# Optimization experiments

Measured on AMD Instinct MI355X. Metric: run time of the kernel, lower is better.

## Reference

```python
import jax, jax.numpy as jnp
import numpy as np

N = 100000   # nodes
E = 1600000  # edges
D = 128      # feature dim
C = 32       # n classes (logits dim)
LN_EPS = 1e-5   # torch LayerNorm default eps
LOG_EPS = 1e-9  # numerical floor inside logs


def setup_inputs() -> dict:
    key = jax.random.key(0)
    ks = jax.random.split(key, 8)
    h = jax.random.normal(ks[0], (N, D), jnp.float32)
    logits = jax.random.normal(ks[1], (N, C), jnp.float32)
    old_z = jax.random.uniform(ks[2], (N,), jnp.float32)
    norm = jax.random.uniform(ks[3], (N, 1), jnp.float32)  # degree norm per node
    tau_1 = jax.random.uniform(ks[4], (1,), jnp.float32)
    tau_2 = jax.random.uniform(ks[5], (1,), jnp.float32)
    src = jax.random.randint(ks[6], (E,), 0, N, jnp.int32)
    dst = jax.random.randint(ks[7], (E,), 0, N, jnp.int32)
    return dict(h=h, logits=logits, old_z=old_z, norm=norm,
                tau_1=tau_1, tau_2=tau_2, src=src, dst=dst)


def _layernorm_over_nodes(x):
    # LayerNorm(N, elementwise_affine=False) applied to a length-N vector:
    # normalize over the entire node dimension.
    mu = jnp.mean(x)
    var = jnp.mean(jnp.square(x - mu))
    return (x - mu) * jax.lax.rsqrt(var + LN_EPS)


def reference(h, logits, old_z, norm, tau_1, tau_2, src, dst):
    # --- message pass 1: adaptive_reduce_func over neighbor logits ---
    probs = jax.nn.softmax(logits, axis=-1)                      # [N,C]
    ones = jnp.ones((src.shape[0],), h.dtype)
    deg = jax.ops.segment_sum(ones, dst, num_segments=N)          # in-degree [N]
    sum_p = jax.ops.segment_sum(probs[src], dst, num_segments=N)  # [N,C]
    mean_p = sum_p / jnp.maximum(deg, 1.0)[:, None]               # neighborhood consensus
    log_self = jnp.log(probs + LOG_EPS)
    log_mean = jnp.log(mean_p + LOG_EPS)
    f1 = jnp.sum(probs * (log_self - log_mean), axis=-1)          # KL(self || mean-neighbor)
    f2 = -jnp.sum(mean_p * log_mean, axis=-1)                     # entropy of consensus
    has_nb = deg > 0  # DGL leaves zero-in-degree nodes at 0
    f1 = jnp.where(has_nb, f1, 0.0)
    f2 = jnp.where(has_nb, f2, 0.0)

    # --- gating (shared_tau=True path) ---
    z = jax.nn.sigmoid(-(_layernorm_over_nodes(f1) - tau_1)) \
      * jax.nn.sigmoid(-(_layernorm_over_nodes(f2) - tau_2))      # [N]
    gate = jnp.minimum(old_z, z)

    # --- message pass 2: sum-aggregate neighbor features ---
    agg = jax.ops.segment_sum(h[src], dst, num_segments=N)        # [N,D]
    normagg = jax.nn.relu(agg * norm)
    new_h = h + gate[:, None] * normagg
    return new_h, z
```

## Files before the change

### kernel.cpp

```cpp
#include <hip/hip_runtime.h>
#include <math.h>

#define CN 32
#define DN 128
#define BKT_SHIFT 9
#define BKT_NODES 512
#define CHUNK 8192
#define MAXBKT 1024
#define DCAP 12288

__global__ void k_softmax(const float* __restrict__ logits, float* __restrict__ probs, int N) {
    int t = blockIdx.x * blockDim.x + threadIdx.x;
    int node = t >> 5, c = t & 31;
    if (node >= N) return;
    float l = logits[node * CN + c];
    float m = l;
    #pragma unroll
    for (int o = 16; o; o >>= 1) m = fmaxf(m, __shfl_xor(m, o, 32));
    float e = __expf(l - m);
    float s = e;
    #pragma unroll
    for (int o = 16; o; o >>= 1) s += __shfl_xor(s, o, 32);
    probs[node * CN + c] = e / s;
}

__global__ void k_part_hist(const int* __restrict__ dst, int* __restrict__ M,
                            int E, int NBKT) {
    __shared__ int hist[MAXBKT];
    int t = threadIdx.x;
    for (int j = t; j < NBKT; j += 256) hist[j] = 0;
    __syncthreads();
    int ebeg = blockIdx.x * CHUNK;
    #pragma unroll
    for (int k = 0; k < CHUNK / 256; ++k) {
        int e = ebeg + k * 256 + t;
        if (e < E) atomicAdd(&hist[dst[e] >> BKT_SHIFT], 1);
    }
    __syncthreads();
    int* row = M + (size_t)blockIdx.x * NBKT;
    for (int j = t; j < NBKT; j += 256) row[j] = hist[j];
}

__global__ void k_part_scan(int* __restrict__ M, int* __restrict__ bbase,
                            int NCH, int NBKT, int E) {
    __shared__ int wsum[16], wpre[16];
    __shared__ int carry;
    int t = threadIdx.x, ln = t & 63, wv = t >> 6;
    if (t == 0) carry = 0;
    __syncthreads();
    int L = NCH * NBKT;
    for (int base = 0; base < L; base += 1024) {
        int k = base + t;
        int idx = 0, v = 0;
        if (k < L) {
            int b = k / NCH, ch = k - b * NCH;
            idx = ch * NBKT + b;
            v = M[idx];
        }
        int incl = v;
        #pragma unroll
        for (int o = 1; o < 64; o <<= 1) { int u = __shfl_up(incl, o, 64); if (ln >= o) incl += u; }
        if (ln == 63) wsum[wv] = incl;
        __syncthreads();
        if (t == 0) {
            int r = carry;
            #pragma unroll
            for (int w = 0; w < 16; ++w) { wpre[w] = r; r += wsum[w]; }
            carry = r;
        }
        __syncthreads();
        if (k < L) M[idx] = wpre[wv] + incl - v;
        __syncthreads();
    }
    for (int b = t; b < NBKT; b += 1024) bbase[b] = M[b];
    if (t == 0) bbase[NBKT] = E;
}

__global__ void k_part_scatter(const int* __restrict__ src, const int* __restrict__ dst,
                               const int* __restrict__ M, int* __restrict__ part,
                               int E, int NBKT) {
    __shared__ int cur[MAXBKT];
    int t = threadIdx.x;
    const int* row = M + (size_t)blockIdx.x * NBKT;
    for (int j = t; j < NBKT; j += 256) cur[j] = row[j];
    __syncthreads();
    int ebeg = blockIdx.x * CHUNK;
    #pragma unroll
    for (int k = 0; k < CHUNK / 256; ++k) {
        int e = ebeg + k * 256 + t;
        if (e < E) {
            int d = dst[e];
            int b = d >> BKT_SHIFT;
            int p = atomicAdd(&cur[b], 1);
            part[p] = ((d & (BKT_NODES - 1)) << 17) | src[e];
        }
    }
}

__global__ void k_bucket_csr(int* __restrict__ part, const int* __restrict__ bbase,
                             int* __restrict__ cnt, int* __restrict__ off, int N) {
    __shared__ int sbuf[DCAP];
    __shared__ int hcnt[BKT_NODES];
    __shared__ int wsum[8], wpre[8];
    int t = threadIdx.x, ln = t & 63, wv = t >> 6;
    int b = blockIdx.x;
    int lo = bbase[b], hi = bbase[b + 1];
    int n = hi - lo;
    if (n > DCAP) n = DCAP;
    for (int e = t; e < n; e += BKT_NODES) sbuf[e] = part[lo + e];
    hcnt[t] = 0;
    __syncthreads();
    for (int e = t; e < n; e += BKT_NODES) atomicAdd(&hcnt[sbuf[e] >> 17], 1);
    __syncthreads();
    int v = hcnt[t];
    int incl = v;
    #pragma unroll
    for (int o = 1; o < 64; o <<= 1) { int u = __shfl_up(incl, o, 64); if (ln >= o) incl += u; }
    if (ln == 63) wsum[wv] = incl;
    __syncthreads();
    if (t == 0) {
        int r = 0;
        #pragma unroll
        for (int w = 0; w < 8; ++w) { wpre[w] = r; r += wsum[w]; }
    }
    __syncthreads();
    int excl = wpre[wv] + incl - v;
    int g = b * BKT_NODES + t;
    if (g < N) { cnt[g] = v; off[g] = lo + excl; }
    hcnt[t] = excl;
    __syncthreads();
    for (int e = t; e < n; e += BKT_NODES) {
        int pk = sbuf[e];
        int p = atomicAdd(&hcnt[pk >> 17], 1);
        part[lo + p] = pk & 0x1FFFF;
    }
}

__global__ void k_fused(const float* __restrict__ probs, const int* __restrict__ off,
                        const int* __restrict__ cnt, const int* __restrict__ eidx,
                        float* __restrict__ f1buf, float* __restrict__ f2buf,
                        double* __restrict__ pbuf,
                        const float* __restrict__ h, float* __restrict__ aggout,
                        int N, int NBF) {
    if ((int)blockIdx.x < NBF) {
        int t = blockIdx.x * blockDim.x + threadIdx.x;
        int i = t >> 5, c = t & 31;
        float f1 = 0.f, f2 = 0.f;
        if (i < N) {
            int beg = off[i], dg = cnt[i];
            float sum = 0.f;
            for (int base = 0; base < dg; base += 16) {
                int rem = dg - base;
                int lim = rem < 16 ? rem : 16;
                int myi = (c < lim) ? eidx[beg + base + c] : 0;
                #pragma unroll
                for (int j = 0; j < 16; ++j) {
                    int s = __shfl(myi, j, 32);
                    float v = probs[(size_t)s * CN + c];
                    sum += (j < rem) ? v : 0.f;
                }
            }
            float f1c = 0.f, f2c = 0.f;
            if (dg > 0) {
                float p = probs[(size_t)i * CN + c];
                float mp = sum / (float)dg;
                float lm = logf(mp + 1e-9f);
                f1c = p * (logf(p + 1e-9f) - lm);
                f2c = -mp * lm;
            }
            #pragma unroll
            for (int o = 16; o; o >>= 1) { f1c += __shfl_xor(f1c, o, 32); f2c += __shfl_xor(f2c, o, 32); }
            if (c == 0) { f1buf[i] = f1c; f2buf[i] = f2c; f1 = f1c; f2 = f2c; }
        }
        double v0 = f1, v1 = (double)f1 * f1, v2 = f2, v3 = (double)f2 * f2;
        #pragma unroll
        for (int o = 32; o; o >>= 1) {
            v0 += __shfl_down(v0, o, 64);
            v1 += __shfl_down(v1, o, 64);
            v2 += __shfl_down(v2, o, 64);
            v3 += __shfl_down(v3, o, 64);
        }
        __shared__ double sh[4][4];
        int wave = threadIdx.x >> 6, lane = threadIdx.x & 63;
        if (lane == 0) { sh[0][wave] = v0; sh[1][wave] = v1; sh[2][wave] = v2; sh[3][wave] = v3; }
        __syncthreads();
        if (threadIdx.x == 0) {
            double a = 0, b = 0, c2 = 0, d = 0;
            #pragma unroll
            for (int w = 0; w < 4; ++w) { a += sh[0][w]; b += sh[1][w]; c2 += sh[2][w]; d += sh[3][w]; }
            double* p = pbuf + (size_t)blockIdx.x * 4;
            p[0] = a; p[1] = b; p[2] = c2; p[3] = d;
        }
    } else {
        int bb = blockIdx.x - NBF;
        int t = bb * blockDim.x + threadIdx.x;
        int i = t >> 6, ln = t & 63;
        if (i >= N) return;
        int beg = off[i], dg = cnt[i];
        const float2* h2 = (const float2*)h;
        float ax = 0.f, ay = 0.f;
        for (int base = 0; base < dg; base += 16) {
            int rem = dg - base;
            int lim = rem < 16 ? rem : 16;
            int myi = (ln < lim) ? eidx[beg + base + ln] : 0;
            #pragma unroll
            for (int j = 0; j < 16; ++j) {
                int s = __shfl(myi, j, 64);
                float2 v = h2[(size_t)s * 64 + ln];
                bool use = j < rem;
                ax += use ? v.x : 0.f;
                ay += use ? v.y : 0.f;
            }
        }
        float2 r; r.x = ax; r.y = ay;
        ((float2*)aggout)[(size_t)i * 64 + ln] = r;
    }
}

__global__ void k_redstats(const double* __restrict__ pbuf, double* __restrict__ stats, int nblk) {
    int t = threadIdx.x;
    double a = 0, b = 0, c = 0, d = 0;
    for (int k = t; k < nblk; k += blockDim.x) {
        const double* p = pbuf + (size_t)k * 4;
        a += p[0]; b += p[1]; c += p[2]; d += p[3];
    }
    #pragma unroll
    for (int o = 32; o; o >>= 1) {
        a += __shfl_down(a, o, 64);
        b += __shfl_down(b, o, 64);
        c += __shfl_down(c, o, 64);
        d += __shfl_down(d, o, 64);
    }
    __shared__ double sh[4][16];
    int wv = t >> 6, ln = t & 63;
    if (ln == 0) { sh[0][wv] = a; sh[1][wv] = b; sh[2][wv] = c; sh[3][wv] = d; }
    __syncthreads();
    if (t == 0) {
        double s0 = 0, s1 = 0, s2 = 0, s3 = 0;
        int nw = blockDim.x >> 6;
        for (int w = 0; w < nw; ++w) { s0 += sh[0][w]; s1 += sh[1][w]; s2 += sh[2][w]; s3 += sh[3][w]; }
        stats[0] = s0; stats[1] = s1; stats[2] = s2; stats[3] = s3;
    }
}

__global__ void k_z_ep(const float* __restrict__ f1buf, const float* __restrict__ f2buf,
                       const double* __restrict__ stats, const float* __restrict__ old_z,
                       const float* __restrict__ tau1, const float* __restrict__ tau2,
                       const float* __restrict__ h, const float* __restrict__ norm,
                       float* __restrict__ out, float* __restrict__ z_out, int N) {
    int t = blockIdx.x * blockDim.x + threadIdx.x;
    int i = t >> 5, c = t & 31;
    if (i >= N) return;
    double invN = 1.0 / (double)N;
    float mu1 = (float)(stats[0] * invN);
    float var1 = (float)(stats[1] * invN) - mu1 * mu1;
    float is1 = rsqrtf(var1 + 1e-5f);
    float mu2 = (float)(stats[2] * invN);
    float var2 = (float)(stats[3] * invN) - mu2 * mu2;
    float is2 = rsqrtf(var2 + 1e-5f);
    float a = (f1buf[i] - mu1) * is1;
    float b = (f2buf[i] - mu2) * is2;
    float z = (1.f / (1.f + __expf(a - tau1[0]))) * (1.f / (1.f + __expf(b - tau2[0])));
    if (c == 0) z_out[i] = z;
    float g = fminf(old_z[i], z);
    float nm = norm[i];
    float4 av = ((const float4*)out)[(size_t)i * 32 + c];
    float4 hv = ((const float4*)h)[(size_t)i * 32 + c];
    float4 r;
    r.x = hv.x + g * fmaxf(av.x * nm, 0.f);
    r.y = hv.y + g * fmaxf(av.y * nm, 0.f);
    r.z = hv.z + g * fmaxf(av.z * nm, 0.f);
    r.w = hv.w + g * fmaxf(av.w * nm, 0.f);
    ((float4*)out)[(size_t)i * 32 + c] = r;
}

extern "C" void kernel_launch(void* const* d_in, const int* in_sizes, int n_in,
                              void* d_out, int out_size, void* d_ws, size_t ws_size,
                              hipStream_t stream) {
    const float* h      = (const float*)d_in[0];
    const float* logits = (const float*)d_in[1];
    const float* old_z  = (const float*)d_in[2];
    const float* norm   = (const float*)d_in[3];
    const float* tau1   = (const float*)d_in[4];
    const float* tau2   = (const float*)d_in[5];
    const int*   src    = (const int*)d_in[6];
    const int*   dst    = (const int*)d_in[7];
    const int N = in_sizes[2];
    const int E = in_sizes[6];

    float* out   = (float*)d_out;
    float* z_out = out + (size_t)N * DN;

    const int B = 256;
    const int NBF  = (N * CN + B - 1) / B;
    const int NG   = (N * 64 + B - 1) / B;
    const int NBKT = (N + BKT_NODES - 1) >> BKT_SHIFT;
    const int NCH  = (E + CHUNK - 1) / CHUNK;

    char*   ws    = (char*)d_ws;
    double* stats = (double*)ws;
    int*    cnt   = (int*)(ws + 64);
    int*    off   = cnt + N;
    int*    bbase = off + N;
    int*    M     = bbase + MAXBKT + 8;
    int*    eidx  = M + (size_t)NCH * NBKT;
    float*  probs = (float*)(eidx + E);
    float*  f1buf = probs + (size_t)N * CN;
    float*  f2buf = f1buf + N;
    double* pbuf  = (double*)(((size_t)(f2buf + N) + 15) & ~(size_t)15);

    k_softmax<<<(N * CN + B - 1) / B, B, 0, stream>>>(logits, probs, N);

    k_part_hist<<<NCH, 256, 0, stream>>>(dst, M, E, NBKT);
    k_part_scan<<<1, 1024, 0, stream>>>(M, bbase, NCH, NBKT, E);
    k_part_scatter<<<NCH, 256, 0, stream>>>(src, dst, M, eidx, E, NBKT);
    k_bucket_csr<<<NBKT, BKT_NODES, 0, stream>>>(eidx, bbase, cnt, off, N);

    k_fused<<<NBF + NG, B, 0, stream>>>(probs, off, cnt, eidx, f1buf, f2buf, pbuf,
                                        h, out, N, NBF);
    k_redstats<<<1, 1024, 0, stream>>>(pbuf, stats, NBF);
    k_z_ep<<<(N * 32 + B - 1) / B, B, 0, stream>>>(f1buf, f2buf, stats, old_z, tau1, tau2,
                                                   h, norm, out, z_out, N);
}
```

Before: 309.3 us.

## Fuse softmax into histogram, parallelize partition scan, column-slice feature gather

Softmax blocks are merged into the histogram kernel launch, removing one launch. The single-block serial scan over the chunk-by-bucket matrix becomes a two-level scan: one block per bucket, then a small scan of bucket totals, with the base offset added in the scatter kernel. The feature aggregation is reorganised so each node is handled by 16-lane groups over four column slices, with those blocks scheduled before the KL blocks, and eidx loads and aggregate stores use nontemporal hints. This cuts the serial scan latency and changes the gather access pattern, at the cost of reloading the index list once per slice.

```diff
diff --git a/kernel.cpp b/kernel.cpp
--- a/kernel.cpp
+++ b/kernel.cpp
@@ -8,81 +8,86 @@
 #define CHUNK 8192
 #define MAXBKT 1024
 #define DCAP 12288
-
-__global__ void k_softmax(const float* __restrict__ logits, float* __restrict__ probs, int N) {
-    int t = blockIdx.x * blockDim.x + threadIdx.x;
-    int node = t >> 5, c = t & 31;
-    if (node >= N) return;
-    float l = logits[node * CN + c];
-    float m = l;
-    #pragma unroll
-    for (int o = 16; o; o >>= 1) m = fmaxf(m, __shfl_xor(m, o, 32));
-    float e = __expf(l - m);
-    float s = e;
-    #pragma unroll
-    for (int o = 16; o; o >>= 1) s += __shfl_xor(s, o, 32);
-    probs[node * CN + c] = e / s;
-}
-
-__global__ void k_part_hist(const int* __restrict__ dst, int* __restrict__ M,
-                            int E, int NBKT) {
-    __shared__ int hist[MAXBKT];
-    int t = threadIdx.x;
-    for (int j = t; j < NBKT; j += 256) hist[j] = 0;
-    __syncthreads();
-    int ebeg = blockIdx.x * CHUNK;
-    #pragma unroll
-    for (int k = 0; k < CHUNK / 256; ++k) {
-        int e = ebeg + k * 256 + t;
-        if (e < E) atomicAdd(&hist[dst[e] >> BKT_SHIFT], 1);
-    }
-    __syncthreads();
-    int* row = M + (size_t)blockIdx.x * NBKT;
-    for (int j = t; j < NBKT; j += 256) row[j] = hist[j];
-}
-
-__global__ void k_part_scan(int* __restrict__ M, int* __restrict__ bbase,
-                            int NCH, int NBKT, int E) {
-    __shared__ int wsum[16], wpre[16];
-    __shared__ int carry;
+#define NSLICE 4
+
+__global__ void k_sm_hist(const int* __restrict__ dst, int* __restrict__ M,
+                          const float* __restrict__ logits, float* __restrict__ probs,
+                          int E, int NBKT, int NCH, int N) {
+    if ((int)blockIdx.x < NCH) {
+        __shared__ int hist[MAXBKT];
+        int t = threadIdx.x;
+        for (int j = t; j < NBKT; j += 256) hist[j] = 0;
+        __syncthreads();
+        int ebeg = blockIdx.x * CHUNK;
+        #pragma unroll
+        for (int k = 0; k < CHUNK / 256; ++k) {
+            int e = ebeg + k * 256 + t;
+            if (e < E) atomicAdd(&hist[dst[e] >> BKT_SHIFT], 1);
+        }
+        __syncthreads();
+        int* row = M + (size_t)blockIdx.x * NBKT;
+        for (int j = t; j < NBKT; j += 256) row[j] = hist[j];
+    } else {
+        int t = (blockIdx.x - NCH) * blockDim.x + threadIdx.x;
+        int node = t >> 5, c = t & 31;
+        if (node >= N) return;
+        float l = logits[node * CN + c];
+        float m = l;
+        #pragma unroll
+        for (int o = 16; o; o >>= 1) m = fmaxf(m, __shfl_xor(m, o, 32));
+        float e = __expf(l - m);
+        float s = e;
+        #pragma unroll
+        for (int o = 16; o; o >>= 1) s += __shfl_xor(s, o, 32);
+        probs[node * CN + c] = e / s;
+    }
+}
+
+__global__ void k_scan_a(int* __restrict__ M, int* __restrict__ bsum, int NCH, int NBKT) {
+    int b = blockIdx.x;
     int t = threadIdx.x, ln = t & 63, wv = t >> 6;
-    if (t == 0) carry = 0;
-    __syncthreads();
-    int L = NCH * NBKT;
-    for (int base = 0; base < L; base += 1024) {
-        int k = base + t;
-        int idx = 0, v = 0;
-        if (k < L) {
-            int b = k / NCH, ch = k - b * NCH;
-            idx = ch * NBKT + b;
-            v = M[idx];
-        }
-        int incl = v;
-        #pragma unroll
-        for (int o = 1; o < 64; o <<= 1) { int u = __shfl_up(incl, o, 64); if (ln >= o) incl += u; }
-        if (ln == 63) wsum[wv] = incl;
-        __syncthreads();
-        if (t == 0) {
-            int r = carry;
-            #pragma unroll
-            for (int w = 0; w < 16; ++w) { wpre[w] = r; r += wsum[w]; }
-            carry = r;
-        }
-        __syncthreads();
-        if (k < L) M[idx] = wpre[wv] + incl - v;
-        __syncthreads();
-    }
-    for (int b = t; b < NBKT; b += 1024) bbase[b] = M[b];
+    int v = (t < NCH) ? M[(size_t)t * NBKT + b] : 0;
+    int incl = v;
+    #pragma unroll
+    for (int o = 1; o < 64; o <<= 1) { int u = __shfl_up(incl, o, 64); if (ln >= o) incl += u; }
+    __shared__ int wsum[4], wpre[4];
+    if (ln == 63) wsum[wv] = incl;
+    __syncthreads();
+    if (t == 0) {
+        int r = 0;
+        for (int w = 0; w < 4; ++w) { wpre[w] = r; r += wsum[w]; }
+    }
+    __syncthreads();
+    int excl = wpre[wv] + incl - v;
+    if (t < NCH) M[(size_t)t * NBKT + b] = excl;
+    if (t == 255) bsum[b] = excl + v;
+}
+
+__global__ void k_scan_b(const int* __restrict__ bsum, int* __restrict__ bbase, int NBKT, int E) {
+    int t = threadIdx.x, ln = t & 63, wv = t >> 6;
+    int v = (t < NBKT) ? bsum[t] : 0;
+    int incl = v;
+    #pragma unroll
+    for (int o = 1; o < 64; o <<= 1) { int u = __shfl_up(incl, o, 64); if (ln >= o) incl += u; }
+    __shared__ int wsum[4], wpre[4];
+    if (ln == 63) wsum[wv] = incl;
+    __syncthreads();
+    if (t == 0) {
+        int r = 0;
+        for (int w = 0; w < 4; ++w) { wpre[w] = r; r += wsum[w]; }
+    }
+    __syncthreads();
+    if (t < NBKT) bbase[t] = wpre[wv] + incl - v;
     if (t == 0) bbase[NBKT] = E;
 }
 
 __global__ void k_part_scatter(const int* __restrict__ src, const int* __restrict__ dst,
-                               const int* __restrict__ M, int* __restrict__ part,
-                               int E, int NBKT) {
+                               const int* __restrict__ M, const int* __restrict__ bbase,
+                               int* __restrict__ part, int E, int NBKT) {
     __shared__ int cur[MAXBKT];
     int t = threadIdx.x;
     const int* row = M + (size_t)blockIdx.x * NBKT;
-    for (int j = t; j < NBKT; j += 256) cur[j] = row[j];
+    for (int j = t; j < NBKT; j += 256) cur[j] = row[j] + bbase[j];
     __syncthreads();
     int ebeg = blockIdx.x * CHUNK;
     #pragma unroll
@@ -141,9 +146,36 @@
                         float* __restrict__ f1buf, float* __restrict__ f2buf,
                         double* __restrict__ pbuf,
                         const float* __restrict__ h, float* __restrict__ aggout,
-                        int N, int NBF) {
-    if ((int)blockIdx.x < NBF) {
-        int t = blockIdx.x * blockDim.x + threadIdx.x;
+                        int N, int NGS, int NBF) {
+    const int HB = NSLICE * NGS;
+    if ((int)blockIdx.x < HB) {
+        int slice = blockIdx.x / NGS;
+        int g = (blockIdx.x - slice * NGS) * 16 + (threadIdx.x >> 4);
+        int c = threadIdx.x & 15;
+        if (g >= N) return;
+        int beg = off[g], dg = cnt[g];
+        const float2* h2 = (const float2*)h;
+        size_t coloff = (size_t)slice * 16 + c;
+        float ax = 0.f, ay = 0.f;
+        for (int base = 0; base < dg; base += 16) {
+            int rem = dg - base;
+            int lim = rem < 16 ? rem : 16;
+            int myi = (c < lim) ? __builtin_nontemporal_load(&eidx[beg + base + c]) : 0;
+            #pragma unroll
+            for (int j = 0; j < 16; ++j) {
+                int s = __shfl(myi, j, 16);
+                float2 v = h2[(size_t)s * 64 + coloff];
+                bool use = j < rem;
+                ax += use ? v.x : 0.f;
+                ay += use ? v.y : 0.f;
+            }
+        }
+        float* op = (float*)&((float2*)aggout)[(size_t)g * 64 + coloff];
+        __builtin_nontemporal_store(ax, op);
+        __builtin_nontemporal_store(ay, op + 1);
+    } else {
+        int pb = blockIdx.x - HB;
+        int t = pb * blockDim.x + threadIdx.x;
         int i = t >> 5, c = t & 31;
         float f1 = 0.f, f2 = 0.f;
         if (i < N) {
@@ -152,7 +184,7 @@
             for (int base = 0; base < dg; base += 16) {
                 int rem = dg - base;
                 int lim = rem < 16 ? rem : 16;
-                int myi = (c < lim) ? eidx[beg + base + c] : 0;
+                int myi = (c < lim) ? __builtin_nontemporal_load(&eidx[beg + base + c]) : 0;
                 #pragma unroll
                 for (int j = 0; j < 16; ++j) {
                     int s = __shfl(myi, j, 32);
@@ -188,32 +220,9 @@
             double a = 0, b = 0, c2 = 0, d = 0;
             #pragma unroll
             for (int w = 0; w < 4; ++w) { a += sh[0][w]; b += sh[1][w]; c2 += sh[2][w]; d += sh[3][w]; }
-            double* p = pbuf + (size_t)blockIdx.x * 4;
+            double* p = pbuf + (size_t)pb * 4;
             p[0] = a; p[1] = b; p[2] = c2; p[3] = d;
         }
-    } else {
-        int bb = blockIdx.x - NBF;
-        int t = bb * blockDim.x + threadIdx.x;
-        int i = t >> 6, ln = t & 63;
-        if (i >= N) return;
-        int beg = off[i], dg = cnt[i];
-        const float2* h2 = (const float2*)h;
-        float ax = 0.f, ay = 0.f;
-        for (int base = 0; base < dg; base += 16) {
-            int rem = dg - base;
-            int lim = rem < 16 ? rem : 16;
-            int myi = (ln < lim) ? eidx[beg + base + ln] : 0;
-            #pragma unroll
-            for (int j = 0; j < 16; ++j) {
-                int s = __shfl(myi, j, 64);
-                float2 v = h2[(size_t)s * 64 + ln];
-                bool use = j < rem;
-                ax += use ? v.x : 0.f;
-                ay += use ? v.y : 0.f;
-            }
-        }
-        float2 r; r.x = ax; r.y = ay;
-        ((float2*)aggout)[(size_t)i * 64 + ln] = r;
     }
 }
 
@@ -293,7 +302,7 @@
 
     const int B = 256;
     const int NBF  = (N * CN + B - 1) / B;
-    const int NG   = (N * 64 + B - 1) / B;
+    const int NGS  = (N + 15) / 16;
     const int NBKT = (N + BKT_NODES - 1) >> BKT_SHIFT;
     const int NCH  = (E + CHUNK - 1) / CHUNK;
 
@@ -302,22 +311,22 @@
     int*    cnt   = (int*)(ws + 64);
     int*    off   = cnt + N;
     int*    bbase = off + N;
-    int*    M     = bbase + MAXBKT + 8;
+    int*    bsum  = bbase + MAXBKT + 8;
+    int*    M     = bsum + MAXBKT;
     int*    eidx  = M + (size_t)NCH * NBKT;
     float*  probs = (float*)(eidx + E);
     float*  f1buf = probs + (size_t)N * CN;
     float*  f2buf = f1buf + N;
     double* pbuf  = (double*)(((size_t)(f2buf + N) + 15) & ~(size_t)15);
 
-    k_softmax<<<(N * CN + B - 1) / B, B, 0, stream>>>(logits, probs, N);
-
-    k_part_hist<<<NCH, 256, 0, stream>>>(dst, M, E, NBKT);
-    k_part_scan<<<1, 1024, 0, stream>>>(M, bbase, NCH, NBKT, E);
-    k_part_scatter<<<NCH, 256, 0, stream>>>(src, dst, M, eidx, E, NBKT);
+    k_sm_hist<<<NCH + NBF, B, 0, stream>>>(dst, M, logits, probs, E, NBKT, NCH, N);
+    k_scan_a<<<NBKT, 256, 0, stream>>>(M, bsum, NCH, NBKT);
+    k_scan_b<<<1, 256, 0, stream>>>(bsum, bbase, NBKT, E);
+    k_part_scatter<<<NCH, 256, 0, stream>>>(src, dst, M, bbase, eidx, E, NBKT);
     k_bucket_csr<<<NBKT, BKT_NODES, 0, stream>>>(eidx, bbase, cnt, off, N);
 
-    k_fused<<<NBF + NG, B, 0, stream>>>(probs, off, cnt, eidx, f1buf, f2buf, pbuf,
-                                        h, out, N, NBF);
+    k_fused<<<NSLICE * NGS + NBF, B, 0, stream>>>(probs, off, cnt, eidx, f1buf, f2buf, pbuf,
+                                                  h, out, N, NGS, NBF);
     k_redstats<<<1, 1024, 0, stream>>>(pbuf, stats, NBF);
     k_z_ep<<<(N * 32 + B - 1) / B, B, 0, stream>>>(f1buf, f2buf, stats, old_z, tau1, tau2,
                                                    h, norm, out, z_out, N);
```

Measured after the change: 249.0 us. 19.5% less time.
